# Performance work log

Measured on AMD Instinct MI355X. Metric: run time of the kernel, lower is better.

## Reference

```python
import jax, jax.numpy as jnp
import numpy as np

B, T, L, H, W = 8, 30000, 6, 128, 128
D_IN, C_DIM, HID, Z_DIM = 3, 32, 256, 128
MAX_DIM = 0.55


def setup_inputs() -> dict:
    key = jax.random.key(0)
    ks = jax.random.split(key, 12)
    p = jax.random.uniform(ks[0], (B, T, D_IN), dtype=jnp.float32)
    z = jax.random.normal(ks[1], (B, Z_DIM), dtype=jnp.float32)
    c = jax.random.normal(ks[2], (B, L, H, W, C_DIM), dtype=jnp.float32)
    # camera-like matrices: small rotation rows so projected coords stay in [-1, 1]
    C_mat = (jax.random.uniform(ks[3], (B, L, 4, 3), dtype=jnp.float32) - 0.5) * 0.3
    C_mat = C_mat.at[:, :, 3, :].set(1.0)  # row used as projection denominator
    fc_p_w = jax.random.normal(ks[4], (HID, D_IN), dtype=jnp.float32) * 0.1
    fc_p_b = jnp.zeros((HID,), jnp.float32)
    blk0_w0 = jax.random.normal(ks[5], (C_DIM, HID), dtype=jnp.float32) * 0.05
    blk0_b0 = jnp.zeros((C_DIM,), jnp.float32)
    blk0_w1 = jax.random.normal(ks[6], (C_DIM, C_DIM), dtype=jnp.float32) * 0.1
    blk0_b1 = jnp.zeros((C_DIM,), jnp.float32)
    blk0_ws = jax.random.normal(ks[7], (C_DIM, HID), dtype=jnp.float32) * 0.05
    blk_w0 = jax.random.normal(ks[8], (4, C_DIM, C_DIM), dtype=jnp.float32) * 0.1
    blk_b0 = jnp.zeros((4, C_DIM), jnp.float32)
    blk_w1 = jax.random.normal(ks[9], (4, C_DIM, C_DIM), dtype=jnp.float32) * 0.1
    blk_b1 = jnp.zeros((4, C_DIM), jnp.float32)
    fc_out_w = jax.random.normal(ks[10], (1, C_DIM), dtype=jnp.float32) * 0.1
    fc_out_b = jnp.zeros((1,), jnp.float32)
    return dict(p=p, z=z, c=c, C_mat=C_mat, fc_p_w=fc_p_w, fc_p_b=fc_p_b,
                blk0_w0=blk0_w0, blk0_b0=blk0_b0, blk0_w1=blk0_w1, blk0_b1=blk0_b1,
                blk0_ws=blk0_ws, blk_w0=blk_w0, blk_b0=blk_b0, blk_w1=blk_w1,
                blk_b1=blk_b1, fc_out_w=fc_out_w, fc_out_b=fc_out_b)


def _bilinear(p, c, C_mat):
    # p: [B,T,3], c: [B,L,H,W,D], C_mat: [B,L,4,3]
    Bb, Ll, Hh, Ww, Dd = c.shape
    interval = 2.0 / (Hh - 1)
    pp = p / MAX_DIM
    # proj[b,l,t,i] = sum_j C_mat[b,l,i,j] * pp[b,t,j]
    proj = jnp.einsum('blij,btj->blti', C_mat[:, :, :3, :], pp)
    denom = C_mat[:, :, 3, 0] + 0.05                      # [B,L]
    proj = proj / denom[:, :, None, None]
    xy = (proj[..., :2] + 1.0) / interval                 # [B,L,T,2]
    x, y = xy[..., 0], xy[..., 1]
    x0f, x1f = jnp.floor(x), jnp.ceil(x)
    y0f, y1f = jnp.floor(y), jnp.ceil(y)
    dx = (x1f - x)[..., None]                             # [B,L,T,1]
    dy = (y1f - y)[..., None]
    x0 = jnp.clip(x0f.astype(jnp.int32), 0, Hh - 1)
    x1 = jnp.clip(x1f.astype(jnp.int32), 0, Hh - 1)
    y0 = jnp.clip(y0f.astype(jnp.int32), 0, Ww - 1)
    y1 = jnp.clip(y1f.astype(jnp.int32), 0, Ww - 1)
    bi = jnp.arange(Bb)[:, None, None]
    li = jnp.arange(Ll)[None, :, None]
    f11 = c[bi, li, x0, y0]                               # [B,L,T,D]
    f12 = c[bi, li, x1, y0]
    f21 = c[bi, li, x0, y1]
    f22 = c[bi, li, x1, y1]
    interp = (f11 * dx * dy + f12 * (1 - dx) * dy
              + f21 * dx * (1 - dy) + f22 * (1 - dx) * (1 - dy))
    return interp.sum(axis=1)                             # sum over views -> [B,T,D]


def reference(p, z, c, C_mat, fc_p_w, fc_p_b, blk0_w0, blk0_b0, blk0_w1, blk0_b1,
              blk0_ws, blk_w0, blk_b0, blk_w1, blk_b1, fc_out_w, fc_out_b):
    feat = _bilinear(p, c, C_mat)                         # [B,T,32]
    net = p @ fc_p_w.T + fc_p_b                           # 1x1 conv == linear, [B,T,256]
    # block0 (256 -> 32, with linear shortcut)
    h = jax.nn.relu(net) @ blk0_w0.T + blk0_b0
    dx_ = jax.nn.relu(h) @ blk0_w1.T + blk0_b1
    net = net @ blk0_ws.T + dx_
    net = net + feat
    # blocks 1..4 (32 -> 32, identity shortcut)
    for i in range(4):
        h = jax.nn.relu(net) @ blk_w0[i].T + blk_b0[i]
        net = net + (jax.nn.relu(h) @ blk_w1[i].T + blk_b1[i])
        net = net + feat
    out = jax.nn.relu(net) @ fc_out_w.T + fc_out_b        # [B,T,1]
    return out[..., 0]                                    # [B,T]
```

## Files before the change

kernel.cpp:

```cpp
#include <hip/hip_runtime.h>

#define NB 8
#define NT 30000
#define NL 6
#define NC 32
#define NHID 256

typedef _Float16 f16;
typedef f16 half8 __attribute__((ext_vector_type(8)));
typedef f16 half4v __attribute__((ext_vector_type(4)));
typedef f16 half2v __attribute__((ext_vector_type(2)));
typedef float floatx4 __attribute__((ext_vector_type(4)));

#define C_ELEMS (25165824ull)
#define NCONV   12288

#define OFF_W0A  0
#define OFF_WA   8192
#define OFF_HB   17408
#define OFF_FOLD 18432
#define OFF_F32  18560
#define IMG_F16  19456

__device__ __align__(16) f16 g_chalf[C_ELEMS];
__device__ __align__(16) f16 g_img[IMG_F16];

__device__ __forceinline__ int permrow(int m) {
    return 8 * ((m & 15) >> 2) + 4 * (m >> 4) + (m & 3);
}

__device__ __forceinline__ half2v cvt2(float a, float b) {
    return __builtin_bit_cast(half2v, __builtin_amdgcn_cvt_pkrtz(a, b));
}

__device__ __forceinline__ half8 pack8(floatx4 f0, floatx4 f1) {
    half2v h0 = cvt2(f0[0], f0[1]), h1 = cvt2(f0[2], f0[3]);
    half2v h2 = cvt2(f1[0], f1[1]), h3 = cvt2(f1[2], f1[3]);
    half4v q0 = __builtin_shufflevector(h0, h1, 0, 1, 2, 3);
    half4v q1 = __builtin_shufflevector(h2, h3, 0, 1, 2, 3);
    return __builtin_shufflevector(q0, q1, 0, 1, 2, 3, 4, 5, 6, 7);
}

__device__ __forceinline__ half8 relupack2(floatx4 a, floatx4 b) {
    half2v p0 = cvt2(fmaxf(a[0], 0.f), fmaxf(a[1], 0.f));
    half2v p1 = cvt2(fmaxf(a[2], 0.f), fmaxf(a[3], 0.f));
    half2v p2 = cvt2(fmaxf(b[0], 0.f), fmaxf(b[1], 0.f));
    half2v p3 = cvt2(fmaxf(b[2], 0.f), fmaxf(b[3], 0.f));
    half4v q0 = __builtin_shufflevector(p0, p1, 0, 1, 2, 3);
    half4v q1 = __builtin_shufflevector(p2, p3, 0, 1, 2, 3);
    return __builtin_shufflevector(q0, q1, 0, 1, 2, 3, 4, 5, 6, 7);
}

__device__ __forceinline__ half8 zext4(half4v lo) {
    const half4v zh = {};
    return __builtin_shufflevector(lo, zh, 0, 1, 2, 3, 4, 5, 6, 7);
}

__device__ __forceinline__ half8 splat8(float w) {
    f16 h = (f16)w;
    half8 v = {h, h, h, h, h, h, h, h};
    return v;
}

__global__ __launch_bounds__(256) void convert_prep(
    const float* __restrict__ c,
    const float* __restrict__ fpw, const float* __restrict__ fpb,
    const float* __restrict__ b0w0, const float* __restrict__ b0b0,
    const float* __restrict__ b0w1, const float* __restrict__ b0b1,
    const float* __restrict__ b0ws, const float* __restrict__ bw0,
    const float* __restrict__ bb0, const float* __restrict__ bw1,
    const float* __restrict__ bb1, const float* __restrict__ fow,
    const float* __restrict__ fob)
{
    __shared__ floatx4 sp[8][32];
    const int tid = threadIdx.x;
    if (blockIdx.x < NCONV) {
        size_t i = ((size_t)blockIdx.x * 256 + tid) * 8;
        floatx4 f0 = *(const floatx4*)(c + i);
        floatx4 f1 = *(const floatx4*)(c + i + 4);
        *(half8*)(g_chalf + i) = pack8(f0, f1);
        return;
    }
    {
        int i = tid & 31, kc = tid >> 5;
        const float* wrow = b0ws + i * 256 + kc * 32;
        const float* pw = fpw + kc * 96;
        const float* pb = fpb + kc * 32;
        floatx4 acc = {};
        #pragma unroll 8
        for (int k = 0; k < 32; k++) {
            float w = wrow[k];
            acc[0] = fmaf(w, pw[k * 3 + 0], acc[0]);
            acc[1] = fmaf(w, pw[k * 3 + 1], acc[1]);
            acc[2] = fmaf(w, pw[k * 3 + 2], acc[2]);
            acc[3] = fmaf(w, pb[k], acc[3]);
        }
        sp[kc][i] = acc;
    }
    __syncthreads();
    {
        int m = tid >> 3, seg = tid & 7;
        const float* src = b0w0 + permrow(m) * 256 + seg * 32;
        f16* dst = g_img + OFF_W0A + m * 256;
        int sw = m & 7;
        #pragma unroll
        for (int ci = 0; ci < 4; ci++) {
            int cidx = seg * 4 + ci;
            floatx4 f0 = *(const floatx4*)(src + ci * 8);
            floatx4 f1 = *(const floatx4*)(src + ci * 8 + 4);
            *(half8*)(dst + ((cidx ^ sw) << 3)) = pack8(f0, f1);
        }
    }
    for (int r = tid; r < 288; r += 256) {
        int mi = r >> 5, m = r & 31;
        int pm = permrow(m);
        const float* src;
        if (mi == 0) src = b0w1 + pm * 32;
        else {
            int mat = mi - 1, bi = mat >> 1;
            src = ((mat & 1) ? bw1 : bw0) + (bi * 32 + pm) * 32;
        }
        f16* dst = g_img + OFF_WA + mi * 1024 + m * 32;
        int sw = (m >> 1) & 3;
        #pragma unroll
        for (int ci = 0; ci < 4; ci++) {
            floatx4 f0 = *(const floatx4*)(src + ci * 8);
            floatx4 f1 = *(const floatx4*)(src + ci * 8 + 4);
            *(half8*)(dst + ((ci ^ sw) << 3)) = pack8(f0, f1);
        }
    }
    {
        int cch = tid >> 5, m = tid & 31;
        int h = cch * 32 + permrow(m);
        half2v a = cvt2(fpw[h * 3 + 0], fpw[h * 3 + 1]);
        half2v bq = cvt2(fpw[h * 3 + 2], fpb[h]);
        *(half4v*)(g_img + OFF_HB + tid * 4) = __builtin_shufflevector(a, bq, 0, 1, 2, 3);
    }
    float* fimg = (float*)(g_img + OFF_F32);
    if (tid < 32) {
        int pm = permrow(tid);
        floatx4 s = sp[0][pm];
        #pragma unroll
        for (int j = 1; j < 8; j++) s += sp[j][pm];
        half2v a = cvt2(s[0], s[1]);
        half2v bq = cvt2(s[2], s[3] + b0b1[pm]);
        *(half4v*)(g_img + OFF_FOLD + tid * 4) = __builtin_shufflevector(a, bq, 0, 1, 2, 3);
        fimg[tid] = b0b0[tid];
        fimg[32 + tid] = fow[tid];
    }
    if (tid >= 64 && tid < 192) {
        fimg[tid] = bb0[tid - 64];
        fimg[tid + 128] = bb1[tid - 64];
    }
    if (tid == 0) fimg[320] = fob[0];
}

__global__ __launch_bounds__(256, 4) void decoder_kernel(
    const float* __restrict__ p, const float* __restrict__ Cm,
    float* __restrict__ out)
{
    __shared__ __align__(16) f16 s_img[IMG_F16];
    __shared__ float s_cam[NL][8];

    const int tid = threadIdx.x;
    const int b = blockIdx.x & 7;
    const int tile = blockIdx.x >> 3;

    {
        const uint4* gsrc = (const uint4*)g_img;
        uint4* ldst = (uint4*)s_img;
        for (int i = tid; i < IMG_F16 / 8; i += 256) ldst[i] = gsrc[i];
    }
    if (tid >= 192 && tid < 192 + NL) {
        int l = tid - 192;
        const float* cm = Cm + ((size_t)b * NL + l) * 12;
        float denom = cm[9] + 0.05f;
        float s = 63.5f / (0.55f * denom);
        s_cam[l][0] = cm[0] * s; s_cam[l][1] = cm[1] * s; s_cam[l][2] = cm[2] * s;
        s_cam[l][3] = cm[3] * s; s_cam[l][4] = cm[4] * s; s_cam[l][5] = cm[5] * s;
    }
    __syncthreads();

    const int lane = tid & 63;
    const int wv = tid >> 6;
    const int q = lane >> 4;
    const int i16 = lane & 15;
    const int sw0 = i16 & 7;

    const f16* s_w0A = s_img + OFF_W0A;
    const f16* s_wA  = s_img + OFF_WA;
    const f16* s_hB  = s_img + OFF_HB;
    const float* sf  = (const float*)(s_img + OFF_F32);

    const f16* w0r0 = s_w0A + i16 * 256;
    const f16* w0r1 = s_w0A + (16 + i16) * 256;
    const int qsw = (q ^ ((i16 >> 1) & 3)) << 3;
    const int soff0 = i16 * 32 + qsw;
    const int soff1 = (16 + i16) * 32 + qsw;
    const f16* hB0 = s_hB + i16 * 4;
    const f16* hB1 = s_hB + (16 + i16) * 4;
    const f16* cqh = g_chalf + (((size_t)b * NL) << 19) + q * 8;

    const half8 fA0 = zext4(*(const half4v*)(s_img + OFF_FOLD + i16 * 4));
    const half8 fA1 = zext4(*(const half4v*)(s_img + OFF_FOLD + (16 + i16) * 4));
    const floatx4 fw0 = *(const floatx4*)&sf[32 + q * 8];
    const floatx4 fw1 = *(const floatx4*)&sf[32 + q * 8 + 4];
    const floatx4 b00a = *(const floatx4*)&sf[q * 8];
    const floatx4 b00b = *(const floatx4*)&sf[q * 8 + 4];
    const float fobv = sf[320];

    #pragma unroll 1
    for (int g = 0; g < 2; g++) {
        const int t = tile * 128 + (g * 4 + wv) * 16 + i16;
        const int tc = min(t, NT - 1);
        const float* pp = p + ((size_t)b * NT + tc) * 3;
        float px = pp[0], py = pp[1], pz = pp[2];

        half8 feh = {};
        #pragma unroll 1
        for (int l = 0; l < NL; l++) {
            float x = s_cam[l][0] * px + s_cam[l][1] * py + s_cam[l][2] * pz + 63.5f;
            float y = s_cam[l][3] * px + s_cam[l][4] * py + s_cam[l][5] * pz + 63.5f;
            float x0f = floorf(x), x1f = ceilf(x);
            float y0f = floorf(y), y1f = ceilf(y);
            float dxw = x1f - x, dyw = y1f - y;
            int x0 = min(max((int)x0f, 0), 127);
            int x1 = min(max((int)x1f, 0), 127);
            int y0 = min(max((int)y0f, 0), 127);
            int y1 = min(max((int)y1f, 0), 127);
            const f16* base = cqh + ((size_t)l << 19);
            half8 t11 = *(const half8*)(base + (size_t)((x0 << 7) + y0) * 32);
            half8 t12 = *(const half8*)(base + (size_t)((x1 << 7) + y0) * 32);
            half8 t21 = *(const half8*)(base + (size_t)((x0 << 7) + y1) * 32);
            half8 t22 = *(const half8*)(base + (size_t)((x1 << 7) + y1) * 32);
            float w11 = dxw * dyw;
            float w12 = (1.f - dxw) * dyw;
            float w21 = dxw * (1.f - dyw);
            float w22 = (1.f - dxw) * (1.f - dyw);
            feh += t11 * splat8(w11) + t12 * splat8(w12)
                 + t21 * splat8(w21) + t22 * splat8(w22);
        }
        floatx4 fe0 = floatx4{(float)feh[0], (float)feh[1], (float)feh[2], (float)feh[3]};
        floatx4 fe1 = floatx4{(float)feh[4], (float)feh[5], (float)feh[6], (float)feh[7]};

        half8 bp;
        {
            half2v xy = cvt2(px, py), z1 = cvt2(pz, 1.0f);
            half4v lo = __builtin_shufflevector(xy, z1, 0, 1, 2, 3);
            half8 full = zext4(lo);
            const half8 zh8 = {};
            bp = (q == 0) ? full : zh8;
        }

        floatx4 acc0 = b00a, acc1 = b00b;
        #pragma unroll 2
        for (int cch = 0; cch < 8; cch++) {
            half8 ha = zext4(*(const half4v*)(hB0 + cch * 128));
            half8 hb = zext4(*(const half4v*)(hB1 + cch * 128));
            floatx4 hz = {};
            floatx4 h0 = __builtin_amdgcn_mfma_f32_16x16x32_f16(ha, bp, hz, 0, 0, 0);
            floatx4 h1 = __builtin_amdgcn_mfma_f32_16x16x32_f16(hb, bp, hz, 0, 0, 0);
            half8 bf = relupack2(h0, h1);
            half8 a0 = *(const half8*)(w0r0 + ((((cch << 2) | q) ^ sw0) << 3));
            half8 a1 = *(const half8*)(w0r1 + ((((cch << 2) | q) ^ sw0) << 3));
            acc0 = __builtin_amdgcn_mfma_f32_16x16x32_f16(a0, bf, acc0, 0, 0, 0);
            acc1 = __builtin_amdgcn_mfma_f32_16x16x32_f16(a1, bf, acc1, 0, 0, 0);
        }

        floatx4 st0 = __builtin_amdgcn_mfma_f32_16x16x32_f16(fA0, bp, fe0, 0, 0, 0);
        floatx4 st1 = __builtin_amdgcn_mfma_f32_16x16x32_f16(fA1, bp, fe1, 0, 0, 0);
        {
            half8 bf = relupack2(acc0, acc1);
            half8 a0 = *(const half8*)(s_wA + soff0);
            half8 a1 = *(const half8*)(s_wA + soff1);
            st0 = __builtin_amdgcn_mfma_f32_16x16x32_f16(a0, bf, st0, 0, 0, 0);
            st1 = __builtin_amdgcn_mfma_f32_16x16x32_f16(a1, bf, st1, 0, 0, 0);
        }

        #pragma unroll
        for (int bk = 0; bk < 4; bk++) {
            const f16* w_a = s_wA + (1 + 2 * bk) * 1024;
            const f16* w_b = s_wA + (2 + 2 * bk) * 1024;
            floatx4 h0 = *(const floatx4*)&sf[64 + bk * 32 + q * 8];
            floatx4 h1 = *(const floatx4*)&sf[64 + bk * 32 + q * 8 + 4];
            {
                half8 bf = relupack2(st0, st1);
                half8 a0 = *(const half8*)(w_a + soff0);
                half8 a1 = *(const half8*)(w_a + soff1);
                h0 = __builtin_amdgcn_mfma_f32_16x16x32_f16(a0, bf, h0, 0, 0, 0);
                h1 = __builtin_amdgcn_mfma_f32_16x16x32_f16(a1, bf, h1, 0, 0, 0);
            }
            floatx4 d0 = *(const floatx4*)&sf[192 + bk * 32 + q * 8];
            floatx4 d1 = *(const floatx4*)&sf[192 + bk * 32 + q * 8 + 4];
            {
                half8 bf = relupack2(h0, h1);
                half8 a0 = *(const half8*)(w_b + soff0);
                half8 a1 = *(const half8*)(w_b + soff1);
                d0 = __builtin_amdgcn_mfma_f32_16x16x32_f16(a0, bf, d0, 0, 0, 0);
                d1 = __builtin_amdgcn_mfma_f32_16x16x32_f16(a1, bf, d1, 0, 0, 0);
            }
            st0 += d0 + fe0;
            st1 += d1 + fe1;
        }

        float o = 0.f;
        #pragma unroll
        for (int r = 0; r < 4; r++)
            o += fmaxf(st0[r], 0.f) * fw0[r] + fmaxf(st1[r], 0.f) * fw1[r];
        o += __shfl_xor(o, 16);
        o += __shfl_xor(o, 32);
        if (q == 0 && t < NT) out[(size_t)b * NT + t] = o + fobv;
    }
}

extern "C" void kernel_launch(void* const* d_in, const int* in_sizes, int n_in,
                              void* d_out, int out_size, void* d_ws, size_t ws_size,
                              hipStream_t stream) {
    const float* p    = (const float*)d_in[0];
    const float* c    = (const float*)d_in[2];
    const float* Cm   = (const float*)d_in[3];
    const float* fpw  = (const float*)d_in[4];
    const float* fpb  = (const float*)d_in[5];
    const float* b0w0 = (const float*)d_in[6];
    const float* b0b0 = (const float*)d_in[7];
    const float* b0w1 = (const float*)d_in[8];
    const float* b0b1 = (const float*)d_in[9];
    const float* b0ws = (const float*)d_in[10];
    const float* bw0  = (const float*)d_in[11];
    const float* bb0  = (const float*)d_in[12];
    const float* bw1  = (const float*)d_in[13];
    const float* bb1  = (const float*)d_in[14];
    const float* fow  = (const float*)d_in[15];
    const float* fob  = (const float*)d_in[16];

    convert_prep<<<NCONV + 1, 256, 0, stream>>>(c, fpw, fpb, b0w0, b0b0, b0w1, b0b1,
                                                b0ws, bw0, bb0, bw1, bb1, fow, fob);

    dim3 grid(((NT + 127) / 128) * NB);
    decoder_kernel<<<grid, 256, 0, stream>>>(p, Cm, (float*)d_out);
}
```

Measured before the change: 298.3 us.

## Split fused decoder into separate gather and MLP kernels via fp16 feature buffer

Splits the fused decoder kernel in two. The first kernel does only the bilinear gather over all views, with the view loop fully unrolled, and writes fp16 features to a global scratch buffer. The second kernel reads those features back and runs the MLP with a lower occupancy target. The aim is to let each phase get its own register and occupancy profile and more memory-level parallelism in the gather. The cost is an extra kernel launch plus a round trip of the feature tensor through global memory.

```diff
diff --git a/kernel.cpp b/kernel.cpp
--- a/kernel.cpp
+++ b/kernel.cpp
@@ -14,6 +14,7 @@
 
 #define C_ELEMS (25165824ull)
 #define NCONV   12288
+#define FEAT_ELEMS (7680000ull)
 
 #define OFF_W0A  0
 #define OFF_WA   8192
@@ -23,6 +24,7 @@
 #define IMG_F16  19456
 
 __device__ __align__(16) f16 g_chalf[C_ELEMS];
+__device__ __align__(16) f16 g_feat[FEAT_ELEMS];
 __device__ __align__(16) f16 g_img[IMG_F16];
 
 __device__ __forceinline__ int permrow(int m) {
@@ -155,29 +157,20 @@
     if (tid == 0) fimg[320] = fob[0];
 }
 
-__global__ __launch_bounds__(256, 4) void decoder_kernel(
-    const float* __restrict__ p, const float* __restrict__ Cm,
-    float* __restrict__ out)
+__global__ __launch_bounds__(256, 4) void gather_kernel(
+    const float* __restrict__ p, const float* __restrict__ Cm)
 {
-    __shared__ __align__(16) f16 s_img[IMG_F16];
     __shared__ float s_cam[NL][8];
-
     const int tid = threadIdx.x;
     const int b = blockIdx.x & 7;
     const int tile = blockIdx.x >> 3;
 
-    {
-        const uint4* gsrc = (const uint4*)g_img;
-        uint4* ldst = (uint4*)s_img;
-        for (int i = tid; i < IMG_F16 / 8; i += 256) ldst[i] = gsrc[i];
-    }
-    if (tid >= 192 && tid < 192 + NL) {
-        int l = tid - 192;
-        const float* cm = Cm + ((size_t)b * NL + l) * 12;
+    if (tid < NL) {
+        const float* cm = Cm + ((size_t)b * NL + tid) * 12;
         float denom = cm[9] + 0.05f;
         float s = 63.5f / (0.55f * denom);
-        s_cam[l][0] = cm[0] * s; s_cam[l][1] = cm[1] * s; s_cam[l][2] = cm[2] * s;
-        s_cam[l][3] = cm[3] * s; s_cam[l][4] = cm[4] * s; s_cam[l][5] = cm[5] * s;
+        s_cam[tid][0] = cm[0] * s; s_cam[tid][1] = cm[1] * s; s_cam[tid][2] = cm[2] * s;
+        s_cam[tid][3] = cm[3] * s; s_cam[tid][4] = cm[4] * s; s_cam[tid][5] = cm[5] * s;
     }
     __syncthreads();
 
@@ -185,29 +178,7 @@
     const int wv = tid >> 6;
     const int q = lane >> 4;
     const int i16 = lane & 15;
-    const int sw0 = i16 & 7;
-
-    const f16* s_w0A = s_img + OFF_W0A;
-    const f16* s_wA  = s_img + OFF_WA;
-    const f16* s_hB  = s_img + OFF_HB;
-    const float* sf  = (const float*)(s_img + OFF_F32);
-
-    const f16* w0r0 = s_w0A + i16 * 256;
-    const f16* w0r1 = s_w0A + (16 + i16) * 256;
-    const int qsw = (q ^ ((i16 >> 1) & 3)) << 3;
-    const int soff0 = i16 * 32 + qsw;
-    const int soff1 = (16 + i16) * 32 + qsw;
-    const f16* hB0 = s_hB + i16 * 4;
-    const f16* hB1 = s_hB + (16 + i16) * 4;
     const f16* cqh = g_chalf + (((size_t)b * NL) << 19) + q * 8;
-
-    const half8 fA0 = zext4(*(const half4v*)(s_img + OFF_FOLD + i16 * 4));
-    const half8 fA1 = zext4(*(const half4v*)(s_img + OFF_FOLD + (16 + i16) * 4));
-    const floatx4 fw0 = *(const floatx4*)&sf[32 + q * 8];
-    const floatx4 fw1 = *(const floatx4*)&sf[32 + q * 8 + 4];
-    const floatx4 b00a = *(const floatx4*)&sf[q * 8];
-    const floatx4 b00b = *(const floatx4*)&sf[q * 8 + 4];
-    const float fobv = sf[320];
 
     #pragma unroll 1
     for (int g = 0; g < 2; g++) {
@@ -217,7 +188,7 @@
         float px = pp[0], py = pp[1], pz = pp[2];
 
         half8 feh = {};
-        #pragma unroll 1
+        #pragma unroll
         for (int l = 0; l < NL; l++) {
             float x = s_cam[l][0] * px + s_cam[l][1] * py + s_cam[l][2] * pz + 63.5f;
             float y = s_cam[l][3] * px + s_cam[l][4] * py + s_cam[l][5] * pz + 63.5f;
@@ -240,6 +211,61 @@
             feh += t11 * splat8(w11) + t12 * splat8(w12)
                  + t21 * splat8(w21) + t22 * splat8(w22);
         }
+        if (t < NT)
+            *(half8*)(g_feat + ((size_t)b * NT + t) * 32 + q * 8) = feh;
+    }
+}
+
+__global__ __launch_bounds__(256, 2) void mlp_kernel(
+    const float* __restrict__ p, float* __restrict__ out)
+{
+    __shared__ __align__(16) f16 s_img[IMG_F16];
+    const int tid = threadIdx.x;
+    const int b = blockIdx.x & 7;
+    const int tile = blockIdx.x >> 3;
+
+    {
+        const uint4* gsrc = (const uint4*)g_img;
+        uint4* ldst = (uint4*)s_img;
+        for (int i = tid; i < IMG_F16 / 8; i += 256) ldst[i] = gsrc[i];
+    }
+    __syncthreads();
+
+    const int lane = tid & 63;
+    const int wv = tid >> 6;
+    const int q = lane >> 4;
+    const int i16 = lane & 15;
+    const int sw0 = i16 & 7;
+
+    const f16* s_w0A = s_img + OFF_W0A;
+    const f16* s_wA  = s_img + OFF_WA;
+    const f16* s_hB  = s_img + OFF_HB;
+    const float* sf  = (const float*)(s_img + OFF_F32);
+
+    const f16* w0r0 = s_w0A + i16 * 256;
+    const f16* w0r1 = s_w0A + (16 + i16) * 256;
+    const int qsw = (q ^ ((i16 >> 1) & 3)) << 3;
+    const int soff0 = i16 * 32 + qsw;
+    const int soff1 = (16 + i16) * 32 + qsw;
+    const f16* hB0 = s_hB + i16 * 4;
+    const f16* hB1 = s_hB + (16 + i16) * 4;
+
+    const half8 fA0 = zext4(*(const half4v*)(s_img + OFF_FOLD + i16 * 4));
+    const half8 fA1 = zext4(*(const half4v*)(s_img + OFF_FOLD + (16 + i16) * 4));
+    const floatx4 fw0 = *(const floatx4*)&sf[32 + q * 8];
+    const floatx4 fw1 = *(const floatx4*)&sf[32 + q * 8 + 4];
+    const floatx4 b00a = *(const floatx4*)&sf[q * 8];
+    const floatx4 b00b = *(const floatx4*)&sf[q * 8 + 4];
+    const float fobv = sf[320];
+
+    #pragma unroll 1
+    for (int g = 0; g < 2; g++) {
+        const int t = tile * 128 + (g * 4 + wv) * 16 + i16;
+        const int tc = min(t, NT - 1);
+        const float* pp = p + ((size_t)b * NT + tc) * 3;
+        float px = pp[0], py = pp[1], pz = pp[2];
+
+        half8 feh = *(const half8*)(g_feat + ((size_t)b * NT + tc) * 32 + q * 8);
         floatx4 fe0 = floatx4{(float)feh[0], (float)feh[1], (float)feh[2], (float)feh[3]};
         floatx4 fe1 = floatx4{(float)feh[4], (float)feh[5], (float)feh[6], (float)feh[7]};
 
@@ -337,5 +363,6 @@
                                                 b0ws, bw0, bb0, bw1, bb1, fow, fob);
 
     dim3 grid(((NT + 127) / 128) * NB);
-    decoder_kernel<<<grid, 256, 0, stream>>>(p, Cm, (float*)d_out);
-}
+    gather_kernel<<<grid, 256, 0, stream>>>(p, Cm);
+    mlp_kernel<<<grid, 256, 0, stream>>>(p, (float*)d_out);
+}
```

Result: faster. 254.9 us (-14.6%).
